# Kernel optimization log

Hardware: AMD Instinct MI355X
Metric: run time of the kernel (lower is better)

The kernel has to match this reference:

```python
import jax, jax.numpy as jnp
import numpy as np

BETA = 0.25

def setup_inputs() -> dict:
    key = jax.random.key(0)
    k1, k2 = jax.random.split(key)
    x = jax.random.normal(k1, (32, 32, 32, 64), dtype=jnp.float32)
    # tf.random_uniform_initializer default: uniform in [-0.05, 0.05]
    embeddings = jax.random.uniform(k2, (64, 1024), dtype=jnp.float32,
                                    minval=-0.05, maxval=0.05)
    return {"x": x, "embeddings": embeddings}

def reference(x, embeddings):
    D, K = embeddings.shape
    flat = x.reshape(-1, D)                                   # [N, D]
    # squared L2 distances to each codebook vector (expanded form)
    sim = flat @ embeddings                                   # [N, K]
    dists = (jnp.sum(flat * flat, axis=1, keepdims=True)
             + jnp.sum(embeddings * embeddings, axis=0)
             - 2.0 * sim)                                     # [N, K]
    idx = jnp.argmin(dists, axis=1)                           # [N]
    quantized = embeddings.T[idx].reshape(x.shape)            # gather == one-hot matmul
    commitment_loss = BETA * jnp.mean((jax.lax.stop_gradient(quantized) - x) ** 2)
    codebook_loss = jnp.mean((quantized - jax.lax.stop_gradient(x)) ** 2)
    loss = commitment_loss + codebook_loss
    out = x + jax.lax.stop_gradient(quantized - x)            # straight-through
    return out, loss
```

## Files before the change

kernel.cpp:

```cpp
#include <hip/hip_runtime.h>
#include <hip/hip_bf16.h>


#define NROWS 32768
#define DDIM  64
#define KCODE 1024
#define NELEM (NROWS * DDIM)
#define MARGIN 4e-3f
#define MAINBLK 256

typedef __attribute__((ext_vector_type(8))) _Float16 f16x8;
typedef __attribute__((ext_vector_type(4))) float f32x4;

static __device__ __forceinline__ unsigned short f2h(float v) {
    _Float16 h = (_Float16)v;
    unsigned short b;
    __builtin_memcpy(&b, &h, 2);
    return b;
}
static __device__ __forceinline__ void gload16(const void* g, void* l) {
    __builtin_amdgcn_global_load_lds(
        (const __attribute__((address_space(1))) void*)g,
        (__attribute__((address_space(3))) void*)l, 16, 0, 0);
}

__global__ void vq_prep(const float* __restrict__ e,
                        float* __restrict__ se,
                        float* __restrict__ eT,
                        unsigned short* __restrict__ ehSw,
                        int* __restrict__ ctrl) {
    __shared__ float tile[64][17];
    const int t = threadIdx.x;
    const int k0 = blockIdx.x * 16;
    if (blockIdx.x == 0 && t < 4) ctrl[t] = 0;
    #pragma unroll
    for (int i = 0; i < 4; ++i) {
        int idx = i * 256 + t;
        int d = idx >> 4, kk = idx & 15;
        tile[d][kk] = e[d * KCODE + k0 + kk];
    }
    __syncthreads();
    if (t < 16) {
        float s = 0.f;
        #pragma unroll
        for (int d = 0; d < 64; ++d) { float v = tile[d][t]; s = fmaf(v, v, s); }
        se[k0 + t] = s;
    }
    const int kk = t >> 4;
    const int dg = (t & 15) * 4;
    const int kg = k0 + kk;
    float v0 = tile[dg + 0][kk], v1 = tile[dg + 1][kk];
    float v2 = tile[dg + 2][kk], v3 = tile[dg + 3][kk];
    *(float4*)&eT[(size_t)kg * 64 + dg] = make_float4(v0, v1, v2, v3);
    const int sw = (((dg >> 3) ^ (kg & 7)) << 3) + (dg & 7);
    *(ushort4*)&ehSw[(size_t)kg * 64 + sw] =
        make_ushort4(f2h(v0), f2h(v1), f2h(v2), f2h(v3));
}

__launch_bounds__(512)
__global__ void vq_main(const float* __restrict__ x,
                        const float* __restrict__ se,
                        const float* __restrict__ eT,
                        const unsigned short* __restrict__ ehSw,
                        float* __restrict__ out,
                        float* __restrict__ parts,
                        int* __restrict__ done) {
    __shared__ unsigned short Beh[KCODE * 64];
    __shared__ float sse[KCODE];
    __shared__ float wsum[8];
    __shared__ float xs[64];
    __shared__ float cb[512];
    __shared__ int   ci[512];
    __shared__ int   flagRows[128];
    __shared__ int   idxRow[128];
    __shared__ int   sNf;
    __shared__ int   lastS;

    const int t = threadIdx.x;
    const int lane = t & 63;
    const int w = t >> 6;
    const int quad = lane >> 4, l15 = lane & 15;
    const int rowBase = blockIdx.x * 128 + w * 16;

    if (t == 0) { sNf = 0; }

    {
        const unsigned char* g = (const unsigned char*)ehSw;
        #pragma unroll
        for (int r = 0; r < 16; ++r)
            gload16(g + (size_t)(r * 512 + t) * 16, &Beh[(r * 512 + t) * 8]);
        float2 s2 = ((const float2*)se)[t];
        sse[2 * t + 0] = s2.x;
        sse[2 * t + 1] = s2.y;
    }

    f16x8 ah0, ah1, al0, al1;
    {
        const float4* ap0 = (const float4*)(x + (size_t)(rowBase + l15) * 64 + quad * 8);
        const float4* ap1 = (const float4*)(x + (size_t)(rowBase + l15) * 64 + 32 + quad * 8);
        float4 a0 = ap0[0], a1 = ap0[1], b0 = ap1[0], b1 = ap1[1];
        float av[8] = {a0.x, a0.y, a0.z, a0.w, a1.x, a1.y, a1.z, a1.w};
        float bv[8] = {b0.x, b0.y, b0.z, b0.w, b1.x, b1.y, b1.z, b1.w};
        f16x8 h0, h1, l0, l1;
        #pragma unroll
        for (int j = 0; j < 8; ++j) {
            _Float16 ha = (_Float16)av[j];
            _Float16 hb = (_Float16)bv[j];
            h0[j] = ha;
            h1[j] = hb;
            l0[j] = (_Float16)(av[j] - (float)ha);
            l1[j] = (_Float16)(bv[j] - (float)hb);
        }
        ah0 = h0; ah1 = h1; al0 = l0; al1 = l1;
    }
    __syncthreads();

    float sb[4], sb2[4];
    int   si[4];
    #pragma unroll
    for (int r = 0; r < 4; ++r) { sb[r] = 3.4e38f; sb2[r] = 3.4e38f; si[r] = 0; }

    const int slot0 = ((quad ^ (l15 & 7)) << 3);
    const int slot1 = (((quad + 4) ^ (l15 & 7)) << 3);

    #pragma unroll 4
    for (int nt = 0; nt < 64; ++nt) {
        const int code = nt * 16 + l15;
        f16x8 b0 = *(const f16x8*)&Beh[code * 64 + slot0];
        f16x8 b1 = *(const f16x8*)&Beh[code * 64 + slot1];
        float cse = sse[code];
        f32x4 aA = {0.f, 0.f, 0.f, 0.f}, aB = {0.f, 0.f, 0.f, 0.f};
        aA = __builtin_amdgcn_mfma_f32_16x16x32_f16(ah0, b0, aA, 0, 0, 0);
        aB = __builtin_amdgcn_mfma_f32_16x16x32_f16(ah1, b1, aB, 0, 0, 0);
        aA = __builtin_amdgcn_mfma_f32_16x16x32_f16(al0, b0, aA, 0, 0, 0);
        aB = __builtin_amdgcn_mfma_f32_16x16x32_f16(al1, b1, aB, 0, 0, 0);
        #pragma unroll
        for (int r = 0; r < 4; ++r) {
            float key = fmaf(-2.f, aA[r] + aB[r], cse);
            bool lt = key < sb[r];
            sb2[r] = fminf(sb2[r], fmaxf(sb[r], key));
            sb[r]  = fminf(sb[r], key);
            si[r]  = lt ? code : si[r];
        }
    }

    #pragma unroll
    for (int m = 1; m < 16; m <<= 1) {
        #pragma unroll
        for (int r = 0; r < 4; ++r) {
            float ob  = __shfl_xor(sb[r],  m, 64);
            float ob2 = __shfl_xor(sb2[r], m, 64);
            int   oi  = __shfl_xor(si[r],  m, 64);
            float nb2 = fminf(fminf(sb2[r], ob2), fmaxf(sb[r], ob));
            bool take = (ob < sb[r]) || (ob == sb[r] && oi < si[r]);
            sb[r] = take ? ob : sb[r];
            si[r] = take ? oi : si[r];
            sb2[r] = nb2;
        }
    }

    if (l15 == 0) {
        #pragma unroll
        for (int r = 0; r < 4; ++r) {
            const int rloc = w * 16 + quad * 4 + r;
            idxRow[rloc] = si[r];
            if (sb2[r] - sb[r] < MARGIN) {
                int p = atomicAdd(&sNf, 1);
                flagRows[p] = rloc;
            }
        }
    }
    __syncthreads();

    const int nf = sNf;
    for (int i = 0; i < nf; ++i) {
        const int rloc = flagRows[i];
        const size_t grow = (size_t)blockIdx.x * 128 + rloc;
        if (t < 64) xs[t] = x[grow * 64 + t];
        __syncthreads();

        float sx = 0.f;
        #pragma unroll
        for (int d = 0; d < 64; ++d) sx = fmaf(xs[d], xs[d], sx);

        const int k0 = t * 2;
        const float4* e0 = (const float4*)(eT + (size_t)(k0 + 0) * 64);
        const float4* e1 = (const float4*)(eT + (size_t)(k0 + 1) * 64);
        float dot0 = 0.f, dot1 = 0.f;
        #pragma unroll
        for (int i4 = 0; i4 < 16; ++i4) {
            float4 v0 = e0[i4], v1 = e1[i4];
            float xa = xs[4 * i4 + 0], xb = xs[4 * i4 + 1];
            float xc = xs[4 * i4 + 2], xd = xs[4 * i4 + 3];
            dot0 = fmaf(xa, v0.x, dot0); dot0 = fmaf(xb, v0.y, dot0);
            dot0 = fmaf(xc, v0.z, dot0); dot0 = fmaf(xd, v0.w, dot0);
            dot1 = fmaf(xa, v1.x, dot1); dot1 = fmaf(xb, v1.y, dot1);
            dot1 = fmaf(xc, v1.z, dot1); dot1 = fmaf(xd, v1.w, dot1);
        }
        float dd0 = (sx + sse[k0 + 0]) - 2.0f * dot0;
        float dd1 = (sx + sse[k0 + 1]) - 2.0f * dot1;
        float db = dd0; int di = k0;
        if (dd1 < db) { db = dd1; di = k0 + 1; }
        cb[t] = db; ci[t] = di;
        __syncthreads();

        if (t < 64) {
            float B = cb[t]; int I = ci[t];
            #pragma unroll
            for (int s = 64; s < 512; s += 64) {
                float b = cb[t + s]; int i2 = ci[t + s];
                bool take = (b < B) || (b == B && i2 < I);
                B = take ? b : B;
                I = take ? i2 : I;
            }
            #pragma unroll
            for (int m = 1; m < 64; m <<= 1) {
                float ob = __shfl_xor(B, m, 64);
                int   oi = __shfl_xor(I, m, 64);
                bool take = (ob < B) || (ob == B && oi < I);
                B = take ? ob : B;
                I = take ? oi : I;
            }
            if (t == 0) idxRow[rloc] = I;
        }
        __syncthreads();
    }

    const int myidx = idxRow[w * 16 + l15];
    {
        const float4* qrow = (const float4*)(eT + (size_t)myidx * 64 + quad * 16);
        const float4* xrow = (const float4*)(x + (size_t)(rowBase + l15) * 64 + quad * 16);
        float4* orow = (float4*)(out + (size_t)(rowBase + l15) * 64 + quad * 16);
        float lsum = 0.f;
        #pragma unroll
        for (int i = 0; i < 4; ++i) {
            float4 q = qrow[i];
            float4 xv = xrow[i];
            float4 o;
            float dx;
            dx = q.x - xv.x; o.x = xv.x + dx; lsum = fmaf(dx, dx, lsum);
            dx = q.y - xv.y; o.y = xv.y + dx; lsum = fmaf(dx, dx, lsum);
            dx = q.z - xv.z; o.z = xv.z + dx; lsum = fmaf(dx, dx, lsum);
            dx = q.w - xv.w; o.w = xv.w + dx; lsum = fmaf(dx, dx, lsum);
            orow[i] = o;
        }
        #pragma unroll
        for (int off = 32; off > 0; off >>= 1)
            lsum += __shfl_down(lsum, off, 64);
        if (lane == 0) wsum[w] = lsum;
    }
    __syncthreads();

    if (t == 0) {
        float s = 0.f;
        #pragma unroll
        for (int i = 0; i < 8; ++i) s += wsum[i];
        __hip_atomic_store(&parts[blockIdx.x], s, __ATOMIC_RELEASE,
                           __HIP_MEMORY_SCOPE_AGENT);
        int fin = __hip_atomic_fetch_add(done, 1, __ATOMIC_ACQ_REL,
                                         __HIP_MEMORY_SCOPE_AGENT);
        lastS = (fin == MAINBLK - 1) ? 1 : 0;
    }
    __syncthreads();
    if (lastS) {
        if (t < 256)
            cb[t] = __hip_atomic_load(&parts[t], __ATOMIC_ACQUIRE,
                                      __HIP_MEMORY_SCOPE_AGENT);
        __syncthreads();
        if (t < 64) {
            float v = cb[t] + cb[t + 64] + cb[t + 128] + cb[t + 192];
            #pragma unroll
            for (int off = 32; off > 0; off >>= 1)
                v += __shfl_down(v, off, 64);
            if (t == 0) {
                float m = v / (float)NELEM;
                out[NELEM] = 0.25f * m + m;
            }
        }
    }
}

extern "C" void kernel_launch(void* const* d_in, const int* in_sizes, int n_in,
                              void* d_out, int out_size, void* d_ws, size_t ws_size,
                              hipStream_t stream) {
    const float* x = (const float*)d_in[0];
    const float* e = (const float*)d_in[1];
    float* out = (float*)d_out;
    float* ws  = (float*)d_ws;

    int*   done          = (int*)(ws + 2);
    float* se            = ws + 64;
    float* eT            = ws + 1280;
    unsigned short* ehSw = (unsigned short*)(ws + 66816);
    float* parts         = ws + 165120;

    vq_prep<<<64, 256, 0, stream>>>(e, se, eT, ehSw, (int*)ws);
    vq_main<<<MAINBLK, 512, 0, stream>>>(x, se, eT, ehSw, out, parts, done);
}
```

Measured before the change: 113.8 us.

## Track top-3 candidates to resolve near-tie rows with cheap two-way exact rescoring

The MFMA scan now keeps the best three distances and the top two code indices per row. Rows whose third-best is also within the margin still go through the full serial 1024-code fp32 rescoring loop. Rows where only the second-best is close are resolved in parallel by computing exact fp32 distances for just the two candidates, two threads per row. This is meant to cut the per-block serial fallback loop with its many barriers, at the cost of more registers and selects in the hot inner loop and a longer shuffle merge.

Result: no change. 114.2 us (+0.3%).

```diff
diff --git a/kernel.cpp b/kernel.cpp
--- a/kernel.cpp
+++ b/kernel.cpp
@@ -71,9 +71,12 @@
     __shared__ float xs[64];
     __shared__ float cb[512];
     __shared__ int   ci[512];
-    __shared__ int   flagRows[128];
+    __shared__ int   lightRows[128];
+    __shared__ int   lightA[128];
+    __shared__ int   lightB[128];
+    __shared__ int   heavyRows[128];
     __shared__ int   idxRow[128];
-    __shared__ int   sNf;
+    __shared__ int   sNl, sNh;
     __shared__ int   lastS;
 
     const int t = threadIdx.x;
@@ -82,7 +85,7 @@
     const int quad = lane >> 4, l15 = lane & 15;
     const int rowBase = blockIdx.x * 128 + w * 16;
 
-    if (t == 0) { sNf = 0; }
+    if (t == 0) { sNl = 0; sNh = 0; }
 
     {
         const unsigned char* g = (const unsigned char*)ehSw;
@@ -115,10 +118,13 @@
     }
     __syncthreads();
 
-    float sb[4], sb2[4];
-    int   si[4];
+    float sb[4], sb2[4], sb3[4];
+    int   si[4], si2[4];
     #pragma unroll
-    for (int r = 0; r < 4; ++r) { sb[r] = 3.4e38f; sb2[r] = 3.4e38f; si[r] = 0; }
+    for (int r = 0; r < 4; ++r) {
+        sb[r] = 3.4e38f; sb2[r] = 3.4e38f; sb3[r] = 3.4e38f;
+        si[r] = 0; si2[r] = 0;
+    }
 
     const int slot0 = ((quad ^ (l15 & 7)) << 3);
     const int slot1 = (((quad + 4) ^ (l15 & 7)) << 3);
@@ -137,10 +143,16 @@
         #pragma unroll
         for (int r = 0; r < 4; ++r) {
             float key = fmaf(-2.f, aA[r] + aB[r], cse);
-            bool lt = key < sb[r];
-            sb2[r] = fminf(sb2[r], fmaxf(sb[r], key));
-            sb[r]  = fminf(sb[r], key);
-            si[r]  = lt ? code : si[r];
+            bool lt1 = key < sb[r];
+            bool lt2 = key < sb2[r];
+            bool lt3 = key < sb3[r];
+            sb3[r] = lt2 ? sb2[r] : (lt3 ? key : sb3[r]);
+            float nsb2 = lt1 ? sb[r] : (lt2 ? key : sb2[r]);
+            int   nsi2 = lt1 ? si[r] : (lt2 ? code : si2[r]);
+            sb[r]  = lt1 ? key  : sb[r];
+            si[r]  = lt1 ? code : si[r];
+            sb2[r] = nsb2;
+            si2[r] = nsi2;
         }
     }
 
@@ -148,14 +160,21 @@
     for (int m = 1; m < 16; m <<= 1) {
         #pragma unroll
         for (int r = 0; r < 4; ++r) {
-            float ob  = __shfl_xor(sb[r],  m, 64);
-            float ob2 = __shfl_xor(sb2[r], m, 64);
-            int   oi  = __shfl_xor(si[r],  m, 64);
-            float nb2 = fminf(fminf(sb2[r], ob2), fmaxf(sb[r], ob));
-            bool take = (ob < sb[r]) || (ob == sb[r] && oi < si[r]);
-            sb[r] = take ? ob : sb[r];
-            si[r] = take ? oi : si[r];
-            sb2[r] = nb2;
+            float b1 = __shfl_xor(sb[r],  m, 64);
+            int   i1 = __shfl_xor(si[r],  m, 64);
+            float b2 = __shfl_xor(sb2[r], m, 64);
+            int   i2 = __shfl_xor(si2[r], m, 64);
+            float b3 = __shfl_xor(sb3[r], m, 64);
+            bool t1 = (b1 < sb[r]) || (b1 == sb[r] && i1 < si[r]);
+            float w1 = t1 ? b1 : sb[r];    int wi1 = t1 ? i1 : si[r];
+            float l1 = t1 ? sb[r] : b1;    int li1 = t1 ? si[r] : i1;
+            float c2 = t1 ? b2 : sb2[r];   int ci2 = t1 ? i2 : si2[r];
+            float c3 = t1 ? b3 : sb3[r];
+            float o2 = t1 ? sb2[r] : b2;
+            bool t2 = (c2 < l1) || (c2 == l1 && ci2 < li1);
+            float w2 = t2 ? c2 : l1;       int wi2 = t2 ? ci2 : li1;
+            float w3 = t2 ? fminf(l1, c3) : fminf(c2, o2);
+            sb[r] = w1; si[r] = wi1; sb2[r] = w2; si2[r] = wi2; sb3[r] = w3;
         }
     }
 
@@ -165,16 +184,48 @@
             const int rloc = w * 16 + quad * 4 + r;
             idxRow[rloc] = si[r];
             if (sb2[r] - sb[r] < MARGIN) {
-                int p = atomicAdd(&sNf, 1);
-                flagRows[p] = rloc;
+                if (sb3[r] - sb[r] < MARGIN) {
+                    int p = atomicAdd(&sNh, 1);
+                    heavyRows[p] = rloc;
+                } else {
+                    int p = atomicAdd(&sNl, 1);
+                    lightRows[p] = rloc;
+                    lightA[p] = si[r];
+                    lightB[p] = si2[r];
+                }
             }
         }
     }
     __syncthreads();
 
-    const int nf = sNf;
-    for (int i = 0; i < nf; ++i) {
-        const int rloc = flagRows[i];
+    const int nl = sNl;
+    const int nh = sNh;
+    if (t < 2 * nl) {
+        const int j = t >> 1, s = t & 1;
+        const int rloc = lightRows[j];
+        const int code = s ? lightB[j] : lightA[j];
+        const float4* xr = (const float4*)(x + ((size_t)blockIdx.x * 128 + rloc) * 64);
+        const float4* er = (const float4*)(eT + (size_t)code * 64);
+        float sx = 0.f, dot = 0.f;
+        #pragma unroll
+        for (int i4 = 0; i4 < 16; ++i4) {
+            float4 xv = xr[i4];
+            float4 ev = er[i4];
+            sx = fmaf(xv.x, xv.x, sx); sx = fmaf(xv.y, xv.y, sx);
+            sx = fmaf(xv.z, xv.z, sx); sx = fmaf(xv.w, xv.w, sx);
+            dot = fmaf(xv.x, ev.x, dot); dot = fmaf(xv.y, ev.y, dot);
+            dot = fmaf(xv.z, ev.z, dot); dot = fmaf(xv.w, ev.w, dot);
+        }
+        float dd = (sx + sse[code]) - 2.0f * dot;
+        float ddo = __shfl_xor(dd, 1, 64);
+        int   ido = __shfl_xor(code, 1, 64);
+        bool take = (ddo < dd) || (ddo == dd && ido < code);
+        int best = take ? ido : code;
+        if (s == 0) idxRow[rloc] = best;
+    }
+
+    for (int i = 0; i < nh; ++i) {
+        const int rloc = heavyRows[i];
         const size_t grow = (size_t)blockIdx.x * 128 + rloc;
         if (t < 64) xs[t] = x[grow * 64 + t];
         __syncthreads();
@@ -225,6 +276,7 @@
         }
         __syncthreads();
     }
+    __syncthreads();
 
     const int myidx = idxRow[w * 16 + l15];
     {
```
